# Optimization experiments

Hardware: AMD Instinct MI355X
Metric: run time of the kernel (lower is better)

The kernel has to match this reference:

```python
import jax, jax.numpy as jnp
import numpy as np

B, S, H = 1, 1024, 2048
E, F, FS = 32, 768, 4096
TOP_K = 4
SCALE = 0.02


def setup_inputs() -> dict:
    key = jax.random.key(0)
    ks = jax.random.split(key, 9)
    return {
        "hidden_states": jax.random.normal(ks[0], (B, S, H), jnp.float32),
        "router_weight": jax.random.normal(ks[1], (E, H), jnp.float32) * SCALE,
        "w_gate": jax.random.normal(ks[2], (E, H, F), jnp.float32) * SCALE,
        "w_up": jax.random.normal(ks[3], (E, H, F), jnp.float32) * SCALE,
        "w_down": jax.random.normal(ks[4], (E, F, H), jnp.float32) * SCALE,
        "sw_gate": jax.random.normal(ks[5], (H, FS), jnp.float32) * SCALE,
        "sw_up": jax.random.normal(ks[6], (H, FS), jnp.float32) * SCALE,
        "sw_down": jax.random.normal(ks[7], (FS, H), jnp.float32) * SCALE,
        "sgate_w": jax.random.normal(ks[8], (H, 1), jnp.float32) * SCALE,
    }


def reference(hidden_states, router_weight, w_gate, w_up, w_down,
              sw_gate, sw_up, sw_down, sgate_w):
    b, s, h = hidden_states.shape
    x = hidden_states.reshape(-1, h)                      # [T,H]
    T = x.shape[0]

    # ---- router: linear -> softmax (fp32) -> topk -> renormalize ----
    logits = x @ router_weight.T                          # [T,E]
    probs = jax.nn.softmax(logits.astype(jnp.float32), axis=-1)
    topv, topi = jax.lax.top_k(probs, TOP_K)              # [T,K]
    topv = topv / jnp.sum(topv, axis=-1, keepdims=True)
    topv = topv.astype(probs.dtype)

    # combine weights: scatter topk weights into dense [T,E] mask
    combine = jnp.zeros((T, E), probs.dtype).at[
        jnp.arange(T)[:, None], topi].add(topv)

    # ---- experts: SwiGLU per expert, weighted combine ----
    g = jnp.einsum('th,ehf->etf', x, w_gate)              # [E,T,F]
    u = jnp.einsum('th,ehf->etf', x, w_up)                # [E,T,F]
    act = jax.nn.silu(g) * u                              # [E,T,F]
    out = jnp.einsum('te,etf,efh->th', combine, act, w_down)  # [T,H]

    # ---- shared expert with sigmoid gate ----
    shared = (jax.nn.silu(x @ sw_gate) * (x @ sw_up)) @ sw_down  # [T,H]
    out = out + jax.nn.sigmoid(x @ sgate_w) * shared

    return out.reshape(b, s, h)
```

## Files before the change

kernel.cpp:

```cpp
#include <hip/hip_runtime.h>
#include <math.h>

#define T_TOK 1024
#define H_DIM 2048
#define N_EXP 32
#define TOPK  4
#define F_DIM 768
#define FS_DIM 4096
#define FS_HALF 2048
#define MAXS 896

typedef __bf16 bf16;
typedef __attribute__((ext_vector_type(4))) __bf16 bf16x4;
typedef __attribute__((ext_vector_type(8))) __bf16 bf16x8;
typedef __attribute__((ext_vector_type(4))) float f32x4;

#define BAR() do {                                        \
    asm volatile("s_waitcnt lgkmcnt(0)" ::: "memory");    \
    __builtin_amdgcn_s_barrier();                         \
    __builtin_amdgcn_sched_barrier(0);                    \
  } while (0)

__device__ __forceinline__ int swz(int row, int colB) {
  return row * 64 + (colB ^ (((row >> 2) & 3) << 4));
}

__global__ __launch_bounds__(256) void router_kernel(
    const float* __restrict__ x, const float* __restrict__ rw,
    const float* __restrict__ sgw,
    float* __restrict__ topw, float* __restrict__ sg,
    int* __restrict__ counts, int* __restrict__ lists)
{
  int t = blockIdx.x; int tid = threadIdx.x;
  int lane = tid & 63, wave = tid >> 6;
  float acc[N_EXP];
  #pragma unroll
  for (int e = 0; e < N_EXP; e++) acc[e] = 0.f;
  float accs = 0.f;
  const float* xr = x + (size_t)t * H_DIM;
  for (int h = tid; h < H_DIM; h += 256) {
    float xv = xr[h];
    accs += xv * sgw[h];
    #pragma unroll
    for (int e = 0; e < N_EXP; e++) acc[e] += xv * rw[e * H_DIM + h];
  }
  __shared__ float red[4][N_EXP];
  __shared__ float reds[4];
  __shared__ float logits[N_EXP];
  #pragma unroll
  for (int e = 0; e < N_EXP; e++) {
    float v = acc[e];
    for (int off = 32; off; off >>= 1) v += __shfl_down(v, off, 64);
    if (lane == 0) red[wave][e] = v;
  }
  {
    float v = accs;
    for (int off = 32; off; off >>= 1) v += __shfl_down(v, off, 64);
    if (lane == 0) reds[wave] = v;
  }
  __syncthreads();
  if (tid < N_EXP) logits[tid] = red[0][tid] + red[1][tid] + red[2][tid] + red[3][tid];
  __syncthreads();
  if (tid == 0) {
    float m = -1e30f;
    #pragma unroll
    for (int e = 0; e < N_EXP; e++) m = fmaxf(m, logits[e]);
    float p[N_EXP];
    #pragma unroll
    for (int e = 0; e < N_EXP; e++) p[e] = expf(logits[e] - m);
    int ids[TOPK]; float vs[TOPK]; float wsum = 0.f;
    #pragma unroll
    for (int k = 0; k < TOPK; k++) {
      int best = 0; float bv = -1.f;
      for (int e = 0; e < N_EXP; e++) {
        if (p[e] > bv) { bv = p[e]; best = e; }
      }
      ids[k] = best; vs[k] = bv; wsum += bv; p[best] = -2.f;
    }
    float inv = 1.f / wsum;
    float sgs = reds[0] + reds[1] + reds[2] + reds[3];
    sg[t] = 1.f / (1.f + expf(-sgs));
    #pragma unroll
    for (int k = 0; k < TOPK; k++) {
      int slot = t * TOPK + k;
      topw[slot] = vs[k] * inv;
      int pos = atomicAdd(&counts[ids[k]], 1);
      lists[ids[k] * T_TOK + pos] = slot;
    }
  }
}

__global__ __launch_bounds__(64) void planner_kernel(
    const int* __restrict__ counts, int* __restrict__ hdr,
    int* __restrict__ gu, int nfb_sh)
{
  int s = threadIdx.x;
  if (s < 8) {
    int n = 0;
    int* dst = gu + s * MAXS;
    for (int f = s; f < nfb_sh; f += 8)
      for (int m = 0; m < T_TOK / 32; m++) dst[n++] = 0x80000000 | (m << 8) | f;
    for (int e = s; e < N_EXP; e += 8) {
      int mg = (counts[e] + 31) >> 5;
      for (int m = 0; m < mg; m++)
        for (int f = 0; f < F_DIM / 128; f++) dst[n++] = (e << 16) | (m << 8) | f;
    }
    hdr[s] = n;
  }
}

__global__ __launch_bounds__(256, 3) void gateup_fused(
    const float* __restrict__ X,
    const float* __restrict__ wg_, const float* __restrict__ wu_,
    const float* __restrict__ swg, const float* __restrict__ swu,
    bf16* __restrict__ act, bf16* __restrict__ acts,
    const int* __restrict__ lists, const int* __restrict__ counts,
    const int* __restrict__ hdr, const int* __restrict__ gu_str,
    int actsN, int col_off, int mode)
{
  int s = blockIdx.x & 7;
  int i = blockIdx.x >> 3;
  if (i >= hdr[s]) return;
  int it = gu_str[s * MAXS + i];
  bool gather = !(it & 0x80000000);
  if (mode == 1 && gather) return;

  const float *Wg, *Wu; const int* lb = nullptr;
  int count, mt, fb, ldb, Nout; bf16* C;
  if (gather) {
    int e = (it >> 16) & 0xff;
    mt = ((it >> 8) & 0xff) * 32; fb = (it & 0xff) * 128;
    count = counts[e]; lb = lists + e * T_TOK;
    Wg = wg_ + (size_t)e * H_DIM * F_DIM;
    Wu = wu_ + (size_t)e * H_DIM * F_DIM;
    ldb = F_DIM; Nout = F_DIM; C = act;
  } else {
    mt = ((it >> 8) & 0xff) * 32; fb = (it & 0xff) * 128;
    count = T_TOK; ldb = FS_DIM; Nout = actsN;
    Wg = swg + col_off; Wu = swu + col_off;
    C = acts;
  }

  __shared__ alignas(16) char sA [2][32 * 64];
  __shared__ alignas(16) char sBg[2][128 * 64];
  __shared__ alignas(16) char sBu[2][128 * 64];

  int tid = threadIdx.x;
  int lane = tid & 63, wid = tid >> 6;
  int wr = wid >> 1, wc = wid & 1;
  int l15 = lane & 15, qB = (lane >> 4) << 4;
  int bng = tid & 31;
  int bk4 = (tid >> 5) << 2;

  const float* aptr;
  {
    int r = mt + (tid >> 3);
    int rc = r < count ? r : count - 1;
    int tok = gather ? (lb[rc] >> 2) : rc;
    aptr = X + (size_t)tok * H_DIM + ((tid & 7) << 2);
  }
  const float* bgp = Wg + (size_t)bk4 * ldb + fb + bng * 4;
  const float* bup = Wu + (size_t)bk4 * ldb + fb + bng * 4;

  f32x4 accg[4], accu[4];
  #pragma unroll
  for (int n = 0; n < 4; n++) {
    accg[n] = (f32x4){0.f,0.f,0.f,0.f};
    accu[n] = (f32x4){0.f,0.f,0.f,0.f};
  }

  f32x4 ava, gva[4], uva[4];
  f32x4 avb, gvb[4], uvb[4];

  #define GU_ISSUE(av, gv, uv, k0) do {                               \
    av = *(const f32x4*)(aptr + (k0));                                \
    _Pragma("unroll")                                                 \
    for (int r_ = 0; r_ < 4; r_++) {                                  \
      gv[r_] = *(const f32x4*)(bgp + (size_t)((k0) + r_) * ldb);      \
      uv[r_] = *(const f32x4*)(bup + (size_t)((k0) + r_) * ldb);      \
    } } while (0)

  #define GU_STAGE(b, av, gv, uv) do {                                \
    bf16x4 ta;                                                        \
    ta[0]=(bf16)av[0]; ta[1]=(bf16)av[1];                             \
    ta[2]=(bf16)av[2]; ta[3]=(bf16)av[3];                             \
    *(bf16x4*)(sA[b] + swz(tid >> 3, (tid & 7) << 3)) = ta;           \
    _Pragma("unroll")                                                 \
    for (int i_ = 0; i_ < 4; i_++) {                                  \
      bf16x4 tg, tu;                                                  \
      tg[0]=(bf16)gva_[0][i_]; tg[1]=(bf16)gva_[1][i_];               \
      tg[2]=(bf16)gva_[2][i_]; tg[3]=(bf16)gva_[3][i_];               \
      tu[0]=(bf16)uva_[0][i_]; tu[1]=(bf16)uva_[1][i_];               \
      tu[2]=(bf16)uva_[2][i_]; tu[3]=(bf16)uva_[3][i_];               \
      *(bf16x4*)(sBg[b] + swz(bng * 4 + i_, bk4 << 1)) = tg;          \
      *(bf16x4*)(sBu[b] + swz(bng * 4 + i_, bk4 << 1)) = tu;          \
    } } while (0)

  #define GU_STAGE2(b, av, gv, uv) { const f32x4* gva_ = gv; const f32x4* uva_ = uv; \
    { f32x4 av_ = av; bf16x4 ta;                                      \
      ta[0]=(bf16)av_[0]; ta[1]=(bf16)av_[1];                         \
      ta[2]=(bf16)av_[2]; ta[3]=(bf16)av_[3];                         \
      *(bf16x4*)(sA[b] + swz(tid >> 3, (tid & 7) << 3)) = ta; }       \
    _Pragma("unroll")                                                 \
    for (int i_ = 0; i_ < 4; i_++) {                                  \
      bf16x4 tg, tu;                                                  \
      tg[0]=(bf16)gva_[0][i_]; tg[1]=(bf16)gva_[1][i_];               \
      tg[2]=(bf16)gva_[2][i_]; tg[3]=(bf16)gva_[3][i_];               \
      tu[0]=(bf16)uva_[0][i_]; tu[1]=(bf16)uva_[1][i_];               \
      tu[2]=(bf16)uva_[2][i_]; tu[3]=(bf16)uva_[3][i_];               \
      *(bf16x4*)(sBg[b] + swz(bng * 4 + i_, bk4 << 1)) = tg;          \
      *(bf16x4*)(sBu[b] + swz(bng * 4 + i_, bk4 << 1)) = tu;          \
    } }

  #define GU_MFMA(b) do {                                             \
    __builtin_amdgcn_s_setprio(1);                                    \
    bf16x8 af = *(const bf16x8*)(sA[b] + swz(wr * 16 + l15, qB));     \
    _Pragma("unroll")                                                 \
    for (int n_ = 0; n_ < 4; n_++) {                                  \
      int rb = wc * 64 + n_ * 16 + l15;                               \
      bf16x8 bg = *(const bf16x8*)(sBg[b] + swz(rb, qB));             \
      bf16x8 bu = *(const bf16x8*)(sBu[b] + swz(rb, qB));             \
      accg[n_] = __builtin_amdgcn_mfma_f32_16x16x32_bf16(af, bg, accg[n_], 0,0,0); \
      accu[n_] = __builtin_amdgcn_mfma_f32_16x16x32_bf16(af, bu, accu[n_], 0,0,0); \
    }                                                                 \
    __builtin_amdgcn_s_setprio(0);                                    \
  } while (0)

  const int NT = H_DIM / 32;
  GU_ISSUE(ava, gva, uva, 0);
  GU_ISSUE(avb, gvb, uvb, 32);
  GU_STAGE2(0, ava, gva, uva);
  GU_ISSUE(ava, gva, uva, 64);
  BAR();
  for (int t = 0; t < NT; t += 2) {
    GU_MFMA(0);
    GU_STAGE2(1, avb, gvb, uvb);
    if (t + 3 < NT) GU_ISSUE(avb, gvb, uvb, (t + 3) * 32);
    BAR();
    GU_MFMA(1);
    if (t + 2 < NT) {
      GU_STAGE2(0, ava, gva, uva);
      if (t + 4 < NT) GU_ISSUE(ava, gva, uva, (t + 4) * 32);
    }
    BAR();
  }
  #undef GU_ISSUE
  #undef GU_STAGE
  #undef GU_STAGE2
  #undef GU_MFMA

  #pragma unroll
  for (int q = 0; q < 4; q++) {
    int gr = mt + wr * 16 + (lane >> 4) * 4 + q;
    if (gr < count) {
      size_t rowo = (gather ? (size_t)lb[gr] : (size_t)gr) * Nout;
      #pragma unroll
      for (int n = 0; n < 4; n++) {
        float g = accg[n][q], u = accu[n][q];
        C[rowo + fb + wc * 64 + n * 16 + l15] =
            (bf16)(g / (1.f + __expf(-g)) * u);
      }
    }
  }
}

__global__ __launch_bounds__(256, 4) void down_fused(
    const bf16* __restrict__ act, const bf16* __restrict__ acts,
    const float* __restrict__ wd_, const float* __restrict__ swd,
    bf16* __restrict__ dslot, float* __restrict__ out,
    const float* __restrict__ sg,
    const int* __restrict__ lists, const int* __restrict__ counts,
    int n_shared, int lda_sh, int kd_sh, int swd_off, int accum)
{
  int id = blockIdx.x;
  bool expert = id >= n_shared;
  const bf16* A; const float* W; const int* lb = nullptr;
  int count, mt, nb, Kd, lda;
  if (expert) {
    int g = id - n_shared;
    int j = g >> 3;
    int e = (g & 7) + 8 * (j >> 7);
    int rr = j & 127;
    nb = (rr & 15) * 128; mt = (rr >> 4) * 64;
    count = counts[e]; lb = lists + e * T_TOK;
    A = act; lda = F_DIM; Kd = F_DIM;
    W = wd_ + (size_t)e * F_DIM * H_DIM;
  } else {
    nb = (id & 15) * 128; mt = (id >> 4) * 64;
    count = T_TOK; A = acts; lda = lda_sh; Kd = kd_sh;
    W = swd + (size_t)swd_off * H_DIM;
  }
  if (mt >= count) return;

  __shared__ alignas(16) char sA[2][64 * 64];
  __shared__ alignas(16) char sB[2][128 * 64];

  int tid = threadIdx.x;
  int lane = tid & 63, wid = tid >> 6;
  int wr = wid >> 1, wc = wid & 1;
  int l15 = lane & 15, qB = (lane >> 4) << 4;
  int bng = tid & 31;
  int bk4 = (tid >> 5) << 2;

  const bf16* aptr;
  {
    int r = mt + (tid >> 2);
    int rc = r < count ? r : count - 1;
    int ar = expert ? lb[rc] : rc;
    aptr = A + (size_t)ar * lda + ((tid & 3) << 3);
  }
  const float* bptr = W + (size_t)bk4 * H_DIM + nb + bng * 4;

  f32x4 acc[2][4];
  #pragma unroll
  for (int m = 0; m < 2; m++)
    #pragma unroll
    for (int n = 0; n < 4; n++)
      acc[m][n] = (f32x4){0.f,0.f,0.f,0.f};

  uint4 ava, avb; f32x4 bva[4], bvb[4];

  #define DN_ISSUE(av, bv, k0) do {                                   \
    av = *(const uint4*)(aptr + (k0));                                \
    _Pragma("unroll")                                                 \
    for (int r_ = 0; r_ < 4; r_++)                                    \
      bv[r_] = *(const f32x4*)(bptr + (size_t)((k0) + r_) * H_DIM);   \
    } while (0)

  #define DN_STAGE(b, av, bv) do {                                    \
    *(uint4*)(sA[b] + swz(tid >> 2, (tid & 3) << 4)) = av;            \
    _Pragma("unroll")                                                 \
    for (int i_ = 0; i_ < 4; i_++) {                                  \
      bf16x4 tb;                                                      \
      tb[0]=(bf16)bv[0][i_]; tb[1]=(bf16)bv[1][i_];                   \
      tb[2]=(bf16)bv[2][i_]; tb[3]=(bf16)bv[3][i_];                   \
      *(bf16x4*)(sB[b] + swz(bng * 4 + i_, bk4 << 1)) = tb;           \
    } } while (0)

  #define DN_MFMA(b) do {                                             \
    __builtin_amdgcn_s_setprio(1);                                    \
    bf16x8 af0 = *(const bf16x8*)(sA[b] + swz(wr * 32 + l15, qB));    \
    bf16x8 af1 = *(const bf16x8*)(sA[b] + swz(wr * 32 + 16 + l15, qB)); \
    _Pragma("unroll")                                                 \
    for (int n_ = 0; n_ < 4; n_++) {                                  \
      bf16x8 bb = *(const bf16x8*)(sB[b] + swz(wc * 64 + n_ * 16 + l15, qB)); \
      acc[0][n_] = __builtin_amdgcn_mfma_f32_16x16x32_bf16(af0, bb, acc[0][n_], 0,0,0); \
      acc[1][n_] = __builtin_amdgcn_mfma_f32_16x16x32_bf16(af1, bb, acc[1][n_], 0,0,0); \
    }                                                                 \
    __builtin_amdgcn_s_setprio(0);                                    \
  } while (0)

  const int NT = Kd / 32;
  DN_ISSUE(ava, bva, 0);
  DN_ISSUE(avb, bvb, 32);
  DN_STAGE(0, ava, bva);
  DN_ISSUE(ava, bva, 64);
  BAR();
  for (int t = 0; t < NT; t += 2) {
    DN_MFMA(0);
    DN_STAGE(1, avb, bvb);
    if (t + 3 < NT) DN_ISSUE(avb, bvb, (t + 3) * 32);
    BAR();
    DN_MFMA(1);
    if (t + 2 < NT) {
      DN_STAGE(0, ava, bva);
      if (t + 4 < NT) DN_ISSUE(ava, bva, (t + 4) * 32);
    }
    BAR();
  }
  #undef DN_ISSUE
  #undef DN_STAGE
  #undef DN_MFMA

  #pragma unroll
  for (int m = 0; m < 2; m++) {
    #pragma unroll
    for (int q = 0; q < 4; q++) {
      int gr = mt + wr * 32 + m * 16 + (lane >> 4) * 4 + q;
      if (gr < count) {
        #pragma unroll
        for (int n = 0; n < 4; n++) {
          int col = nb + wc * 64 + n * 16 + l15;
          if (expert) {
            dslot[(size_t)lb[gr] * H_DIM + col] = (bf16)acc[m][n][q];
          } else if (!accum) {
            out[(size_t)gr * H_DIM + col] = sg[gr] * acc[m][n][q];
          } else {
            out[(size_t)gr * H_DIM + col] += sg[gr] * acc[m][n][q];
          }
        }
      }
    }
  }
}

__global__ __launch_bounds__(256) void combine_kernel(
    const bf16* __restrict__ dslot, const float* __restrict__ topw,
    float* __restrict__ out)
{
  int t = blockIdx.x;
  int h = threadIdx.x * 8;
  float w0 = topw[t * 4 + 0], w1 = topw[t * 4 + 1];
  float w2 = topw[t * 4 + 2], w3 = topw[t * 4 + 3];
  bf16x8 a0 = *(const bf16x8*)&dslot[(size_t)(t * 4 + 0) * H_DIM + h];
  bf16x8 a1 = *(const bf16x8*)&dslot[(size_t)(t * 4 + 1) * H_DIM + h];
  bf16x8 a2 = *(const bf16x8*)&dslot[(size_t)(t * 4 + 2) * H_DIM + h];
  bf16x8 a3 = *(const bf16x8*)&dslot[(size_t)(t * 4 + 3) * H_DIM + h];
  f32x4 o0 = *(f32x4*)&out[(size_t)t * H_DIM + h];
  f32x4 o1 = *(f32x4*)&out[(size_t)t * H_DIM + h + 4];
  float o[8] = {o0[0], o0[1], o0[2], o0[3], o1[0], o1[1], o1[2], o1[3]};
  #pragma unroll
  for (int j = 0; j < 8; j++)
    o[j] += w0 * (float)a0[j] + w1 * (float)a1[j] + w2 * (float)a2[j]
          + w3 * (float)a3[j];
  *(f32x4*)&out[(size_t)t * H_DIM + h]     = (f32x4){o[0], o[1], o[2], o[3]};
  *(f32x4*)&out[(size_t)t * H_DIM + h + 4] = (f32x4){o[4], o[5], o[6], o[7]};
}

extern "C" void kernel_launch(void* const* d_in, const int* in_sizes, int n_in,
                              void* d_out, int out_size, void* d_ws, size_t ws_size,
                              hipStream_t stream) {
  const float* x   = (const float*)d_in[0];
  const float* rw  = (const float*)d_in[1];
  const float* wg  = (const float*)d_in[2];
  const float* wu  = (const float*)d_in[3];
  const float* wd  = (const float*)d_in[4];
  const float* swg = (const float*)d_in[5];
  const float* swu = (const float*)d_in[6];
  const float* swd = (const float*)d_in[7];
  const float* sgw = (const float*)d_in[8];
  float* out = (float*)d_out;
  char* ws = (char*)d_ws;

  bool fullfs = ws_size >= (size_t)32200000;
  size_t actsN = fullfs ? FS_DIM : FS_HALF;
  int nfb_sh = (int)(actsN / 128);
  int sh_per_strand = (nfb_sh / 8) * (T_TOK / 32);

  size_t off = 0;
  int*   counts  = (int*)(ws + off); off += 256;
  int*   hdr     = (int*)(ws + off); off += 64;
  int*   gu_str  = (int*)(ws + off); off += 8 * MAXS * 4;
  int*   lists   = (int*)(ws + off); off += (size_t)N_EXP * T_TOK * 4;
  float* topw    = (float*)(ws + off); off += (size_t)T_TOK * TOPK * 4;
  float* sg      = (float*)(ws + off); off += (size_t)T_TOK * 4;
  bf16*  act     = (bf16*)(ws + off); off += (size_t)T_TOK * TOPK * F_DIM * 2;
  bf16*  acts    = (bf16*)(ws + off); off += (size_t)T_TOK * actsN * 2;
  bf16*  dslot   = (bf16*)(ws + off); off += (size_t)T_TOK * TOPK * H_DIM * 2;

  hipMemsetAsync(counts, 0, 256, stream);

  router_kernel<<<T_TOK, 256, 0, stream>>>(x, rw, sgw, topw, sg, counts, lists);
  planner_kernel<<<1, 64, 0, stream>>>(counts, hdr, gu_str, nfb_sh);

  int gu_grid = 8 * (sh_per_strand + 4 * (T_TOK / 32) * (F_DIM / 128));
  const int DN_EXP = N_EXP * 128;

  if (fullfs) {
    gateup_fused<<<gu_grid, 256, 0, stream>>>(
        x, wg, wu, swg, swu, act, acts, lists, counts, hdr, gu_str,
        FS_DIM, 0, 0);
    down_fused<<<256 + DN_EXP, 256, 0, stream>>>(
        act, acts, wd, swd, dslot, out, sg, lists, counts,
        256, FS_DIM, FS_DIM, 0, 0);
  } else {
    gateup_fused<<<gu_grid, 256, 0, stream>>>(
        x, wg, wu, swg, swu, act, acts, lists, counts, hdr, gu_str,
        FS_HALF, 0, 0);
    down_fused<<<256 + DN_EXP, 256, 0, stream>>>(
        act, acts, wd, swd, dslot, out, sg, lists, counts,
        256, FS_HALF, FS_HALF, 0, 0);
    gateup_fused<<<8 * sh_per_strand, 256, 0, stream>>>(
        x, wg, wu, swg, swu, act, acts, lists, counts, hdr, gu_str,
        FS_HALF, FS_HALF, 1);
    down_fused<<<256, 256, 0, stream>>>(
        act, acts, wd, swd, dslot, out, sg, lists, counts,
        256, FS_HALF, FS_HALF, FS_HALF, 1);
  }
  combine_kernel<<<T_TOK, 256, 0, stream>>>(dslot, topw, out);
}
```

Before: 447.4 us.

## Enlarge gate/up tile to 64 rows with 512 threads, drop planner kernel

The gate/up GEMM kernel moves from 32x128 tiles with 256 threads to 64x128 tiles with 512 threads. The two halves of the block load gate and up weights separately, so each weight tile loaded is reused across twice as many token rows. The planner kernel and its work-list indirection are removed in favour of a static grid in which empty expert tiles exit early. The workspace threshold for the full shared-expert path is also lowered slightly, which may switch which path runs. Risks are many idle blocks for sparsely populated experts, and higher register and LDS use per block, which can lower occupancy.

```diff
diff --git a/kernel.cpp b/kernel.cpp
--- a/kernel.cpp
+++ b/kernel.cpp
@@ -8,7 +8,6 @@
 #define F_DIM 768
 #define FS_DIM 4096
 #define FS_HALF 2048
-#define MAXS 896
 
 typedef __bf16 bf16;
 typedef __attribute__((ext_vector_type(4))) __bf16 bf16x4;
@@ -90,67 +89,44 @@
   }
 }
 
-__global__ __launch_bounds__(64) void planner_kernel(
-    const int* __restrict__ counts, int* __restrict__ hdr,
-    int* __restrict__ gu, int nfb_sh)
-{
-  int s = threadIdx.x;
-  if (s < 8) {
-    int n = 0;
-    int* dst = gu + s * MAXS;
-    for (int f = s; f < nfb_sh; f += 8)
-      for (int m = 0; m < T_TOK / 32; m++) dst[n++] = 0x80000000 | (m << 8) | f;
-    for (int e = s; e < N_EXP; e += 8) {
-      int mg = (counts[e] + 31) >> 5;
-      for (int m = 0; m < mg; m++)
-        for (int f = 0; f < F_DIM / 128; f++) dst[n++] = (e << 16) | (m << 8) | f;
-    }
-    hdr[s] = n;
-  }
-}
-
-__global__ __launch_bounds__(256, 3) void gateup_fused(
+__global__ __launch_bounds__(512, 4) void gateup_fused(
     const float* __restrict__ X,
     const float* __restrict__ wg_, const float* __restrict__ wu_,
     const float* __restrict__ swg, const float* __restrict__ swu,
     bf16* __restrict__ act, bf16* __restrict__ acts,
     const int* __restrict__ lists, const int* __restrict__ counts,
-    const int* __restrict__ hdr, const int* __restrict__ gu_str,
-    int actsN, int col_off, int mode)
+    int n_shared, int sh_nfb, int actsN, int col_off)
 {
-  int s = blockIdx.x & 7;
-  int i = blockIdx.x >> 3;
-  if (i >= hdr[s]) return;
-  int it = gu_str[s * MAXS + i];
-  bool gather = !(it & 0x80000000);
-  if (mode == 1 && gather) return;
-
+  int id = blockIdx.x;
+  bool gather = id >= n_shared;
   const float *Wg, *Wu; const int* lb = nullptr;
   int count, mt, fb, ldb, Nout; bf16* C;
   if (gather) {
-    int e = (it >> 16) & 0xff;
-    mt = ((it >> 8) & 0xff) * 32; fb = (it & 0xff) * 128;
+    int g = id - n_shared;
+    int j = g >> 3;
+    int e = (g & 7) + 8 * (j / 96);
+    int rr = j % 96;
+    mt = (rr / 6) * 64; fb = (rr % 6) * 128;
     count = counts[e]; lb = lists + e * T_TOK;
     Wg = wg_ + (size_t)e * H_DIM * F_DIM;
     Wu = wu_ + (size_t)e * H_DIM * F_DIM;
     ldb = F_DIM; Nout = F_DIM; C = act;
   } else {
-    mt = ((it >> 8) & 0xff) * 32; fb = (it & 0xff) * 128;
+    fb = (id % sh_nfb) * 128; mt = (id / sh_nfb) * 64;
     count = T_TOK; ldb = FS_DIM; Nout = actsN;
     Wg = swg + col_off; Wu = swu + col_off;
     C = acts;
   }
-
-  __shared__ alignas(16) char sA [2][32 * 64];
+  if (mt >= count) return;
+
+  __shared__ alignas(16) char sA [2][64 * 64];
   __shared__ alignas(16) char sBg[2][128 * 64];
   __shared__ alignas(16) char sBu[2][128 * 64];
 
   int tid = threadIdx.x;
   int lane = tid & 63, wid = tid >> 6;
-  int wr = wid >> 1, wc = wid & 1;
+  int wr = wid >> 2, wc = wid & 3;
   int l15 = lane & 15, qB = (lane >> 4) << 4;
-  int bng = tid & 31;
-  int bk4 = (tid >> 5) << 2;
 
   const float* aptr;
   {
@@ -159,106 +135,96 @@
     int tok = gather ? (lb[rc] >> 2) : rc;
     aptr = X + (size_t)tok * H_DIM + ((tid & 7) << 2);
   }
-  const float* bgp = Wg + (size_t)bk4 * ldb + fb + bng * 4;
-  const float* bup = Wu + (size_t)bk4 * ldb + fb + bng * 4;
-
-  f32x4 accg[4], accu[4];
-  #pragma unroll
-  for (int n = 0; n < 4; n++) {
-    accg[n] = (f32x4){0.f,0.f,0.f,0.f};
-    accu[n] = (f32x4){0.f,0.f,0.f,0.f};
-  }
-
-  f32x4 ava, gva[4], uva[4];
-  f32x4 avb, gvb[4], uvb[4];
-
-  #define GU_ISSUE(av, gv, uv, k0) do {                               \
+  int t8 = tid & 255;
+  int bng = t8 & 31;
+  int bk4 = (t8 >> 5) << 2;
+  const float* bptr = (tid < 256 ? Wg : Wu) + (size_t)bk4 * ldb + fb + bng * 4;
+  char* bds = (tid < 256) ? &sBg[0][0] : &sBu[0][0];
+
+  f32x4 accg[2][2], accu[2][2];
+  #pragma unroll
+  for (int m = 0; m < 2; m++)
+    #pragma unroll
+    for (int n = 0; n < 2; n++) {
+      accg[m][n] = (f32x4){0.f,0.f,0.f,0.f};
+      accu[m][n] = (f32x4){0.f,0.f,0.f,0.f};
+    }
+
+  f32x4 ava, bva[4];
+  f32x4 avb, bvb[4];
+
+  #define GU_ISSUE(av, bv, k0) do {                                   \
     av = *(const f32x4*)(aptr + (k0));                                \
     _Pragma("unroll")                                                 \
-    for (int r_ = 0; r_ < 4; r_++) {                                  \
-      gv[r_] = *(const f32x4*)(bgp + (size_t)((k0) + r_) * ldb);      \
-      uv[r_] = *(const f32x4*)(bup + (size_t)((k0) + r_) * ldb);      \
-    } } while (0)
-
-  #define GU_STAGE(b, av, gv, uv) do {                                \
+    for (int r_ = 0; r_ < 4; r_++)                                    \
+      bv[r_] = *(const f32x4*)(bptr + (size_t)((k0) + r_) * ldb);     \
+  } while (0)
+
+  #define GU_STAGE(b, av, bv) do {                                    \
     bf16x4 ta;                                                        \
     ta[0]=(bf16)av[0]; ta[1]=(bf16)av[1];                             \
     ta[2]=(bf16)av[2]; ta[3]=(bf16)av[3];                             \
     *(bf16x4*)(sA[b] + swz(tid >> 3, (tid & 7) << 3)) = ta;           \
     _Pragma("unroll")                                                 \
     for (int i_ = 0; i_ < 4; i_++) {                                  \
-      bf16x4 tg, tu;                                                  \
-      tg[0]=(bf16)gva_[0][i_]; tg[1]=(bf16)gva_[1][i_];               \
-      tg[2]=(bf16)gva_[2][i_]; tg[3]=(bf16)gva_[3][i_];               \
-      tu[0]=(bf16)uva_[0][i_]; tu[1]=(bf16)uva_[1][i_];               \
-      tu[2]=(bf16)uva_[2][i_]; tu[3]=(bf16)uva_[3][i_];               \
-      *(bf16x4*)(sBg[b] + swz(bng * 4 + i_, bk4 << 1)) = tg;          \
-      *(bf16x4*)(sBu[b] + swz(bng * 4 + i_, bk4 << 1)) = tu;          \
+      bf16x4 tb;                                                      \
+      tb[0]=(bf16)bv[0][i_]; tb[1]=(bf16)bv[1][i_];                   \
+      tb[2]=(bf16)bv[2][i_]; tb[3]=(bf16)bv[3][i_];                   \
+      *(bf16x4*)(bds + (b) * (128 * 64) + swz(bng * 4 + i_, bk4 << 1)) = tb; \
     } } while (0)
-
-  #define GU_STAGE2(b, av, gv, uv) { const f32x4* gva_ = gv; const f32x4* uva_ = uv; \
-    { f32x4 av_ = av; bf16x4 ta;                                      \
-      ta[0]=(bf16)av_[0]; ta[1]=(bf16)av_[1];                         \
-      ta[2]=(bf16)av_[2]; ta[3]=(bf16)av_[3];                         \
-      *(bf16x4*)(sA[b] + swz(tid >> 3, (tid & 7) << 3)) = ta; }       \
-    _Pragma("unroll")                                                 \
-    for (int i_ = 0; i_ < 4; i_++) {                                  \
-      bf16x4 tg, tu;                                                  \
-      tg[0]=(bf16)gva_[0][i_]; tg[1]=(bf16)gva_[1][i_];               \
-      tg[2]=(bf16)gva_[2][i_]; tg[3]=(bf16)gva_[3][i_];               \
-      tu[0]=(bf16)uva_[0][i_]; tu[1]=(bf16)uva_[1][i_];               \
-      tu[2]=(bf16)uva_[2][i_]; tu[3]=(bf16)uva_[3][i_];               \
-      *(bf16x4*)(sBg[b] + swz(bng * 4 + i_, bk4 << 1)) = tg;          \
-      *(bf16x4*)(sBu[b] + swz(bng * 4 + i_, bk4 << 1)) = tu;          \
-    } }
 
   #define GU_MFMA(b) do {                                             \
     __builtin_amdgcn_s_setprio(1);                                    \
-    bf16x8 af = *(const bf16x8*)(sA[b] + swz(wr * 16 + l15, qB));     \
-    _Pragma("unroll")                                                 \
-    for (int n_ = 0; n_ < 4; n_++) {                                  \
-      int rb = wc * 64 + n_ * 16 + l15;                               \
+    bf16x8 af0 = *(const bf16x8*)(sA[b] + swz(wr * 32 + l15, qB));    \
+    bf16x8 af1 = *(const bf16x8*)(sA[b] + swz(wr * 32 + 16 + l15, qB)); \
+    _Pragma("unroll")                                                 \
+    for (int n_ = 0; n_ < 2; n_++) {                                  \
+      int rb = wc * 32 + n_ * 16 + l15;                               \
       bf16x8 bg = *(const bf16x8*)(sBg[b] + swz(rb, qB));             \
       bf16x8 bu = *(const bf16x8*)(sBu[b] + swz(rb, qB));             \
-      accg[n_] = __builtin_amdgcn_mfma_f32_16x16x32_bf16(af, bg, accg[n_], 0,0,0); \
-      accu[n_] = __builtin_amdgcn_mfma_f32_16x16x32_bf16(af, bu, accu[n_], 0,0,0); \
+      accg[0][n_] = __builtin_amdgcn_mfma_f32_16x16x32_bf16(af0, bg, accg[0][n_], 0,0,0); \
+      accg[1][n_] = __builtin_amdgcn_mfma_f32_16x16x32_bf16(af1, bg, accg[1][n_], 0,0,0); \
+      accu[0][n_] = __builtin_amdgcn_mfma_f32_16x16x32_bf16(af0, bu, accu[0][n_], 0,0,0); \
+      accu[1][n_] = __builtin_amdgcn_mfma_f32_16x16x32_bf16(af1, bu, accu[1][n_], 0,0,0); \
     }                                                                 \
     __builtin_amdgcn_s_setprio(0);                                    \
   } while (0)
 
   const int NT = H_DIM / 32;
-  GU_ISSUE(ava, gva, uva, 0);
-  GU_ISSUE(avb, gvb, uvb, 32);
-  GU_STAGE2(0, ava, gva, uva);
-  GU_ISSUE(ava, gva, uva, 64);
+  GU_ISSUE(ava, bva, 0);
+  GU_ISSUE(avb, bvb, 32);
+  GU_STAGE(0, ava, bva);
+  GU_ISSUE(ava, bva, 64);
   BAR();
   for (int t = 0; t < NT; t += 2) {
     GU_MFMA(0);
-    GU_STAGE2(1, avb, gvb, uvb);
-    if (t + 3 < NT) GU_ISSUE(avb, gvb, uvb, (t + 3) * 32);
+    GU_STAGE(1, avb, bvb);
+    if (t + 3 < NT) GU_ISSUE(avb, bvb, (t + 3) * 32);
     BAR();
     GU_MFMA(1);
     if (t + 2 < NT) {
-      GU_STAGE2(0, ava, gva, uva);
-      if (t + 4 < NT) GU_ISSUE(ava, gva, uva, (t + 4) * 32);
+      GU_STAGE(0, ava, bva);
+      if (t + 4 < NT) GU_ISSUE(ava, bva, (t + 4) * 32);
     }
     BAR();
   }
   #undef GU_ISSUE
   #undef GU_STAGE
-  #undef GU_STAGE2
   #undef GU_MFMA
 
   #pragma unroll
-  for (int q = 0; q < 4; q++) {
-    int gr = mt + wr * 16 + (lane >> 4) * 4 + q;
-    if (gr < count) {
-      size_t rowo = (gather ? (size_t)lb[gr] : (size_t)gr) * Nout;
-      #pragma unroll
-      for (int n = 0; n < 4; n++) {
-        float g = accg[n][q], u = accu[n][q];
-        C[rowo + fb + wc * 64 + n * 16 + l15] =
-            (bf16)(g / (1.f + __expf(-g)) * u);
+  for (int m = 0; m < 2; m++) {
+    #pragma unroll
+    for (int q = 0; q < 4; q++) {
+      int gr = mt + wr * 32 + m * 16 + (lane >> 4) * 4 + q;
+      if (gr < count) {
+        size_t rowo = (gather ? (size_t)lb[gr] : (size_t)gr) * Nout;
+        #pragma unroll
+        for (int n = 0; n < 2; n++) {
+          float g = accg[m][n][q], u = accu[m][n][q];
+          C[rowo + fb + wc * 32 + n * 16 + l15] =
+              (bf16)(g / (1.f + __expf(-g)) * u);
+        }
       }
     }
   }
@@ -432,15 +398,13 @@
   float* out = (float*)d_out;
   char* ws = (char*)d_ws;
 
-  bool fullfs = ws_size >= (size_t)32200000;
+  bool fullfs = ws_size >= (size_t)32000000;
   size_t actsN = fullfs ? FS_DIM : FS_HALF;
-  int nfb_sh = (int)(actsN / 128);
-  int sh_per_strand = (nfb_sh / 8) * (T_TOK / 32);
+  int sh_nfb = (int)(actsN / 128);
+  int nsh_gu = sh_nfb * (T_TOK / 64);
 
   size_t off = 0;
   int*   counts  = (int*)(ws + off); off += 256;
-  int*   hdr     = (int*)(ws + off); off += 64;
-  int*   gu_str  = (int*)(ws + off); off += 8 * MAXS * 4;
   int*   lists   = (int*)(ws + off); off += (size_t)N_EXP * T_TOK * 4;
   float* topw    = (float*)(ws + off); off += (size_t)T_TOK * TOPK * 4;
   float* sg      = (float*)(ws + off); off += (size_t)T_TOK * 4;
@@ -451,28 +415,27 @@
   hipMemsetAsync(counts, 0, 256, stream);
 
   router_kernel<<<T_TOK, 256, 0, stream>>>(x, rw, sgw, topw, sg, counts, lists);
-  planner_kernel<<<1, 64, 0, stream>>>(counts, hdr, gu_str, nfb_sh);
-
-  int gu_grid = 8 * (sh_per_strand + 4 * (T_TOK / 32) * (F_DIM / 128));
+
+  const int EXP_GU = N_EXP * 96;
   const int DN_EXP = N_EXP * 128;
 
   if (fullfs) {
-    gateup_fused<<<gu_grid, 256, 0, stream>>>(
-        x, wg, wu, swg, swu, act, acts, lists, counts, hdr, gu_str,
-        FS_DIM, 0, 0);
+    gateup_fused<<<nsh_gu + EXP_GU, 512, 0, stream>>>(
+        x, wg, wu, swg, swu, act, acts, lists, counts,
+        nsh_gu, sh_nfb, FS_DIM, 0);
     down_fused<<<256 + DN_EXP, 256, 0, stream>>>(
         act, acts, wd, swd, dslot, out, sg, lists, counts,
         256, FS_DIM, FS_DIM, 0, 0);
   } else {
-    gateup_fused<<<gu_grid, 256, 0, stream>>>(
-        x, wg, wu, swg, swu, act, acts, lists, counts, hdr, gu_str,
-        FS_HALF, 0, 0);
+    gateup_fused<<<nsh_gu + EXP_GU, 512, 0, stream>>>(
+        x, wg, wu, swg, swu, act, acts, lists, counts,
+        nsh_gu, sh_nfb, FS_HALF, 0);
     down_fused<<<256 + DN_EXP, 256, 0, stream>>>(
         act, acts, wd, swd, dslot, out, sg, lists, counts,
         256, FS_HALF, FS_HALF, 0, 0);
-    gateup_fused<<<8 * sh_per_strand, 256, 0, stream>>>(
-        x, wg, wu, swg, swu, act, acts, lists, counts, hdr, gu_str,
-        FS_HALF, FS_HALF, 1);
+    gateup_fused<<<nsh_gu, 512, 0, stream>>>(
+        x, wg, wu, swg, swu, act, acts, lists, counts,
+        nsh_gu, sh_nfb, FS_HALF, FS_HALF);
     down_fused<<<256, 256, 0, stream>>>(
         act, acts, wd, swd, dslot, out, sg, lists, counts,
         256, FS_HALF, FS_HALF, FS_HALF, 1);
```

After: 375.7 us. 16.0% less time.
